# Kernel tuning notes

Hardware: AMD Instinct MI355X
Metric: run time of the kernel (lower is better)

## Reference

```python
import math
import jax, jax.numpy as jnp
import numpy as np

ANCHORS_SETTINGS = (
    dict(layer='p3', stride=32, size=48, scale=[2 ** (1.0 / 3.0), 2 ** (2.0 / 3.0)], aspect_ratio=[0.667, 1, 1.5]),
    dict(layer='p4', stride=64, size=96, scale=[2 ** (1.0 / 3.0), 2 ** (2.0 / 3.0)], aspect_ratio=[0.667, 1, 1.5]),
    dict(layer='p5', stride=128, size=192, scale=[1, 2 ** (1.0 / 3.0), 2 ** (2.0 / 3.0)], aspect_ratio=[0.667, 1, 1.5]),
)


def anchor_configs():
    # 21 static (kernel, stride, padding) configs, in the exact counter order of
    # weighted_anchor_aggregator (p3 x6, p4 x6, p5 x9).
    cfgs = []
    for info in ANCHORS_SETTINGS:
        stride, size = info['stride'], info['size']
        for scale in info['scale']:
            for ar in info['aspect_ratio']:
                kernel = (int(size * scale / float(ar) ** 0.5), int(size * scale * float(ar) ** 0.5))
                padding = (math.ceil((kernel[0] - stride) / 2.0), math.ceil((kernel[1] - stride) / 2.0))
                cfgs.append((kernel, (stride, stride), padding))
    return cfgs


def extract_weighted_patches(x, weights, kernel, stride, padding):
    # x: (B,H,W,C); weights: (B,k,gh,gw). Vectorized equivalent of the original
    # lax.scan over per-position dynamic_slice gathers:
    #   acc = sum_{i,j} weights[:,:,i,j] (x) x_pad[:, i*s : i*s+kh, j*s : j*s+kw, :]
    b = x.shape[0]
    _, k, gh, gw = weights.shape
    xp = jnp.pad(x, ((0, 0),
                     (padding[0], padding[0] + kernel[0]),
                     (padding[1], padding[1] + kernel[1]),
                     (0, 0)))
    rows = jnp.arange(gh)[:, None] * stride[0] + jnp.arange(kernel[0])[None, :]  # (gh, kh)
    cols = jnp.arange(gw)[:, None] * stride[1] + jnp.arange(kernel[1])[None, :]  # (gw, kw)
    # gather all strided patches: (B, gh, kh, gw, kw, C)
    patches = xp[:, rows][:, :, :, cols]
    # weighted sum over grid positions -> (B, k, kh, kw, C)
    return jnp.einsum('bkij,bihjwc->bkhwc', weights, patches)


def _aggregate(x, weights_p3, weights_p4, weights_p5):
    weights = ([weights_p3[:, a] for a in range(weights_p3.shape[1])]
               + [weights_p4[:, a] for a in range(weights_p4.shape[1])]
               + [weights_p5[:, a] for a in range(weights_p5.shape[1])])
    b, k = weights[0].shape[0], weights[0].shape[1]
    acc = jnp.zeros((b * k, 224, 224, 3), x.dtype)
    for w, (kernel, stride, padding) in zip(weights, anchor_configs()):
        agg = extract_weighted_patches(x, w, kernel, stride, padding)
        agg = agg.reshape(b * k, kernel[0], kernel[1], 3)
        acc = acc + jax.image.resize(agg, (b * k, 224, 224, 3), 'bilinear')
    return acc


def setup_inputs() -> dict:
    key = jax.random.key(0)
    k0, k1, k2, k3 = jax.random.split(key, 4)
    B, K = 8, 4
    return {
        'x': jax.random.normal(k0, (B, 448, 448, 3), jnp.float32),
        'weights_p3': jax.random.uniform(k1, (B, 6, K, 14, 14), jnp.float32),
        'weights_p4': jax.random.uniform(k2, (B, 6, K, 7, 7), jnp.float32),
        'weights_p5': jax.random.uniform(k3, (B, 9, K, 4, 4), jnp.float32),
    }


def reference(x, weights_p3, weights_p4, weights_p5):
    return _aggregate(x, weights_p3, weights_p4, weights_p5)
```

## Files before the change

kernel.cpp:

```cpp
#include <hip/hip_runtime.h>
#include <math.h>


#define BATCH 8
#define KK 4
#define OUT_HW 224
#define IMG_HW 448
#define NCFG 21

#define WTBL_BYTES (NCFG * 2 * OUT_HW * 16)
#define ITBL_BYTES (NCFG * 2 * OUT_HW * 4)
#define WT_OFF_BYTES (WTBL_BYTES + ITBL_BYTES)
#define WT_F4 12912
#define AGG_OFF_BYTES (WT_OFF_BYTES + WT_F4 * 16)

#define RZ_GRID (14 * 14 * 16)

typedef float v2f __attribute__((ext_vector_type(2)));

static constexpr int cKH[NCFG]  = {74,60,49,93,76,62, 148,120,98,186,152,124,
                                   235,192,156,296,241,197,373,304,248};
static constexpr int cKW[NCFG]  = {49,60,74,62,76,93, 98,120,148,124,152,186,
                                   156,192,235,197,241,296,248,304,373};
static constexpr int cMTH[NCFG] = {2,2,2,2,2,2, 2,2,2,2,2,2, 3,2,2,3,3,2,4,3,3};
static constexpr int cMTW[NCFG] = {2,2,2,2,2,2, 2,2,2,2,2,2, 2,2,3,2,3,3,3,3,4};

__host__ __device__ constexpr int ckwp(int c) { return cKW[c] + (cKW[c] & 1); }
__host__ __device__ constexpr long cwsoff(int c, int g) {
    long o = 0;
    for (int k = g; k < c; ++k) o += (long)cKH[k] * ckwp(k) * (BATCH * KK);
    return o;
}

struct ACfg {
    int kh, kw, kwp, p0, p1;
    int layer;
    int ns;
    int wt_off;
    int ws_off;
    int block_start;
    int blocks_per_img;
};

struct AggArgs {
    ACfg e[NCFG];
    int n;
};

struct TablesArgs { int kh[NCFG]; int kw[NCFG]; };

struct TrArgs {
    int layer[NCFG];
    int anchor[NCFG];
    int gsz[NCFG];
    int wt_off[NCFG];
};

struct F3 { float a, b, c; };

__device__ inline unsigned int bf16_rne(float f) {
    unsigned int u = __float_as_uint(f);
    return (u + 0x7fffu + ((u >> 16) & 1u)) >> 16;
}

__global__ __launch_bounds__(256) void init_tables(float4* __restrict__ wtbl,
                                                   int* __restrict__ itbl,
                                                   TablesArgs t) {
    int cfg = blockIdx.x >> 1;
    int dim = blockIdx.x & 1;
    int o = threadIdx.x;
    if (o >= OUT_HW) return;
    int n = dim ? t.kw[cfg] : t.kh[cfg];

    float inv = (float)(1.0 / ((double)OUT_HW / (double)n));
    float ks  = inv > 1.f ? inv : 1.f;
    float rks = 1.f / ks;
    float sf  = ((float)o + 0.5f) * inv - 0.5f;
    int i0 = (int)ceilf(sf - ks);  if (i0 < 0) i0 = 0;
    int i1 = (int)floorf(sf + ks); if (i1 > n - 1) i1 = n - 1;
    float sum = 0.f;
    for (int i = i0; i <= i1; ++i) {
        float v = 1.f - fabsf((float)i - sf) * rks;
        sum += (v > 0.f ? v : 0.f);
    }
    float rsum = 1.f / sum;
    float w[4];
#pragma unroll
    for (int d = 0; d < 4; ++d) {
        int i = i0 + d;
        float v = 0.f;
        if (i <= i1) {
            v = 1.f - fabsf((float)i - sf) * rks;
            v = (v > 0.f ? v : 0.f) * rsum;
        }
        w[d] = v;
    }
    int idx = cfg * (2 * OUT_HW) + dim * OUT_HW + o;
    wtbl[idx] = make_float4(w[0], w[1], w[2], w[3]);
    itbl[idx] = i0;
}

__global__ __launch_bounds__(256) void transpose_w(
        const float* __restrict__ wp3, const float* __restrict__ wp4,
        const float* __restrict__ wp5, float4* __restrict__ wT, TrArgs t) {
    int cfg = blockIdx.x;
    int b = blockIdx.y;
    int gsz = t.gsz[cfg];
    const float* base;
    int A;
    if (t.layer[cfg] == 0)      { base = wp3; A = 6; }
    else if (t.layer[cfg] == 1) { base = wp4; A = 6; }
    else                        { base = wp5; A = 9; }
    const float* src = base + (size_t)(b * A + t.anchor[cfg]) * (KK * gsz);
    for (int g = threadIdx.x; g < gsz; g += 256) {
        wT[t.wt_off[cfg] + b * gsz + g] =
            make_float4(src[0 * gsz + g], src[1 * gsz + g],
                        src[2 * gsz + g], src[3 * gsz + g]);
    }
}

template <int GH, int GW, int STRIDE, int L2S>
__device__ inline void agg_body(const ACfg& c, int b, int h, int slot,
                                const float* __restrict__ xb,
                                const float4* __restrict__ wlds,
                                uint2* __restrict__ agg) {
    const int w0 = (((slot >> L2S) << (L2S + 1)) | (slot & (STRIDE - 1)));
    const int w1 = w0 + STRIDE;
    const bool two = w1 < c.kw;

    v2f acc2[4][3];
#pragma unroll
    for (int k = 0; k < 4; ++k)
#pragma unroll
        for (int ch = 0; ch < 3; ++ch) { acc2[k][ch].x = 0.f; acc2[k][ch].y = 0.f; }

    const int rb = h - c.p0;
    int ilo = rb >= 0 ? 0 : (-rb + STRIDE - 1) / STRIDE;
    int ihi = (IMG_HW - 1 - rb) / STRIDE;
    if (ihi > GH - 1) ihi = GH - 1;

    const int cb = w0 - c.p1;

    int  cof[GW + 1];
    bool ok [GW + 1];
#pragma unroll
    for (int jj = 0; jj <= GW; ++jj) {
        int col = cb + jj * STRIDE;
        ok[jj] = (unsigned)col < (unsigned)IMG_HW;
        unsigned cc = (unsigned)col;
        if (cc > (unsigned)(IMG_HW - 1)) cc = (unsigned)(IMG_HW - 1);
        cof[jj] = (int)cc * 3;
    }

#pragma unroll 1
    for (int i = ilo; i <= ihi; ++i) {
        const float* xr = xb + (size_t)(rb + i * STRIDE) * (IMG_HW * 3);
        const float4* wrow = wlds + i * GW;

        float px[GW + 1][3];
#pragma unroll
        for (int jj = 0; jj <= GW; ++jj) {
            F3 v = *(const F3*)(xr + cof[jj]);
            px[jj][0] = ok[jj] ? v.a : 0.f;
            px[jj][1] = ok[jj] ? v.b : 0.f;
            px[jj][2] = ok[jj] ? v.c : 0.f;
        }

#pragma unroll
        for (int j = 0; j < GW; ++j) {
            float4 wk = wrow[j];
            v2f d0 = {px[j][0], px[j + 1][0]};
            v2f d1 = {px[j][1], px[j + 1][1]};
            v2f d2 = {px[j][2], px[j + 1][2]};
            v2f wv0 = {wk.x, wk.x};
            v2f wv1 = {wk.y, wk.y};
            v2f wv2 = {wk.z, wk.z};
            v2f wv3 = {wk.w, wk.w};
            acc2[0][0] = __builtin_elementwise_fma(wv0, d0, acc2[0][0]);
            acc2[0][1] = __builtin_elementwise_fma(wv0, d1, acc2[0][1]);
            acc2[0][2] = __builtin_elementwise_fma(wv0, d2, acc2[0][2]);
            acc2[1][0] = __builtin_elementwise_fma(wv1, d0, acc2[1][0]);
            acc2[1][1] = __builtin_elementwise_fma(wv1, d1, acc2[1][1]);
            acc2[1][2] = __builtin_elementwise_fma(wv1, d2, acc2[1][2]);
            acc2[2][0] = __builtin_elementwise_fma(wv2, d0, acc2[2][0]);
            acc2[2][1] = __builtin_elementwise_fma(wv2, d1, acc2[2][1]);
            acc2[2][2] = __builtin_elementwise_fma(wv2, d2, acc2[2][2]);
            acc2[3][0] = __builtin_elementwise_fma(wv3, d0, acc2[3][0]);
            acc2[3][1] = __builtin_elementwise_fma(wv3, d1, acc2[3][1]);
            acc2[3][2] = __builtin_elementwise_fma(wv3, d2, acc2[3][2]);
        }
    }

    const int npix = c.kh * c.kwp;
    size_t pb0 = (size_t)c.ws_off
               + ((size_t)b * npix + (size_t)h * c.kwp + w0) * KK;
    {
        uint4 s0, s1;
        s0.x = bf16_rne(acc2[0][0].x) | (bf16_rne(acc2[0][1].x) << 16);
        s0.y = bf16_rne(acc2[0][2].x);
        s0.z = bf16_rne(acc2[1][0].x) | (bf16_rne(acc2[1][1].x) << 16);
        s0.w = bf16_rne(acc2[1][2].x);
        s1.x = bf16_rne(acc2[2][0].x) | (bf16_rne(acc2[2][1].x) << 16);
        s1.y = bf16_rne(acc2[2][2].x);
        s1.z = bf16_rne(acc2[3][0].x) | (bf16_rne(acc2[3][1].x) << 16);
        s1.w = bf16_rne(acc2[3][2].x);
        *(uint4*)(agg + pb0)     = s0;
        *(uint4*)(agg + pb0 + 2) = s1;
    }
    if (two) {
        size_t pb1 = pb0 + (size_t)STRIDE * KK;
        uint4 s0, s1;
        s0.x = bf16_rne(acc2[0][0].y) | (bf16_rne(acc2[0][1].y) << 16);
        s0.y = bf16_rne(acc2[0][2].y);
        s0.z = bf16_rne(acc2[1][0].y) | (bf16_rne(acc2[1][1].y) << 16);
        s0.w = bf16_rne(acc2[1][2].y);
        s1.x = bf16_rne(acc2[2][0].y) | (bf16_rne(acc2[2][1].y) << 16);
        s1.y = bf16_rne(acc2[2][2].y);
        s1.z = bf16_rne(acc2[3][0].y) | (bf16_rne(acc2[3][1].y) << 16);
        s1.w = bf16_rne(acc2[3][2].y);
        *(uint4*)(agg + pb1)     = s0;
        *(uint4*)(agg + pb1 + 2) = s1;
    }
}

__device__ inline void agg_top(int bid, const float* __restrict__ x,
                               const float4* __restrict__ wT,
                               uint2* __restrict__ agg, const AggArgs& a,
                               float4* wlds, int tid) {
    int ci = 0;
    while (ci + 1 < a.n && bid >= a.e[ci + 1].block_start) ci++;
    const ACfg c = a.e[ci];
    int local = bid - c.block_start;
    int b     = local & 7;
    int sblk  = local >> 3;

    const int gsz = (c.layer == 0) ? 196 : (c.layer == 1) ? 49 : 16;
    for (int t = tid; t < gsz; t += 256)
        wlds[t] = wT[c.wt_off + b * gsz + t];
    __syncthreads();

    int pidx = sblk * 256 + tid;
    if (pidx >= c.kh * c.ns) return;
    int h    = pidx / c.ns;
    int slot = pidx - h * c.ns;

    const float* __restrict__ xb = x + (size_t)b * (IMG_HW * IMG_HW * 3);
    if (c.layer == 0)      agg_body<14, 14, 32, 5>(c, b, h, slot, xb, wlds, agg);
    else if (c.layer == 1) agg_body<7, 7, 64, 6>(c, b, h, slot, xb, wlds, agg);
    else                   agg_body<4, 4, 128, 7>(c, b, h, slot, xb, wlds, agg);
}

__global__ __launch_bounds__(256, 3) void agg_all(
        const float* __restrict__ x,
        const float4* __restrict__ wT,
        uint2* __restrict__ agg,
        AggArgs a) {
    __shared__ float4 wlds[196];
    agg_top(blockIdx.x, x, wT, agg, a, wlds, (int)threadIdx.x);
}

template <int TH, int TW, int KH_, int KW_, int KWP_>
__device__ inline void taps_ct2(const uint2* __restrict__ pb,
                                int i0, int j0,
                                float4 wh4, float4 ww4,
                                v2f (&a)[3]) {
    const float* wh = (const float*)&wh4;
    const float* ww = (const float*)&ww4;
    uint4 v[TH][TW];
#pragma unroll
    for (int d = 0; d < TH; ++d) {
        int gi = i0 + d;
        if (gi > KH_ - 1) gi = KH_ - 1;
        const uint2* rp = pb + (size_t)gi * (KWP_ * KK);
#pragma unroll
        for (int e = 0; e < TW; ++e) {
            int gj = j0 + e;
            if (gj > KW_ - 1) gj = KW_ - 1;
            v[d][e] = *(const uint4*)(rp + gj * KK);
        }
    }
#pragma unroll
    for (int d = 0; d < TH; ++d) {
        v2f r0 = {0.f, 0.f}, r1 = {0.f, 0.f}, r2 = {0.f, 0.f};
#pragma unroll
        for (int e = 0; e < TW; ++e) {
            uint4 q = v[d][e];
            v2f c0, c1, c2;
            c0.x = __uint_as_float(q.x << 16);
            c0.y = __uint_as_float(q.z << 16);
            c1.x = __uint_as_float(q.x & 0xffff0000u);
            c1.y = __uint_as_float(q.z & 0xffff0000u);
            c2.x = __uint_as_float(q.y << 16);
            c2.y = __uint_as_float(q.w << 16);
            v2f w2 = {ww[e], ww[e]};
            r0 = __builtin_elementwise_fma(w2, c0, r0);
            r1 = __builtin_elementwise_fma(w2, c1, r1);
            r2 = __builtin_elementwise_fma(w2, c2, r2);
        }
        v2f h2 = {wh[d], wh[d]};
        a[0] = __builtin_elementwise_fma(h2, r0, a[0]);
        a[1] = __builtin_elementwise_fma(h2, r1, a[1]);
        a[2] = __builtin_elementwise_fma(h2, r2, a[2]);
    }
}

template <int C, int CEND, int CSTART>
__device__ inline void do_rounds(const uint2* __restrict__ agg,
                                 const float4* __restrict__ wlds,
                                 const int* __restrict__ ilds,
                                 int b, int kp, int tx, int ty,
                                 v2f (&a)[3]) {
    if constexpr (C < CEND) {
        constexpr int li  = C - CSTART;
        constexpr int kh  = cKH[C];
        constexpr int kw  = cKW[C];
        constexpr int kwp = ckwp(C);
        constexpr long wso = cwsoff(C, CSTART);
        float4 wh4 = wlds[li * 32 + ty];
        float4 ww4 = wlds[li * 32 + 16 + tx];
        int i0 = ilds[li * 32 + ty];
        int j0 = ilds[li * 32 + 16 + tx];
        const uint2* pb = agg + wso
                        + (size_t)b * ((size_t)kh * kwp * KK) + kp * 2;
        taps_ct2<cMTH[C], cMTW[C], kh, kw, kwp>(pb, i0, j0, wh4, ww4, a);
        do_rounds<C + 1, CEND, CSTART>(agg, wlds, ilds, b, kp, tx, ty, a);
    }
}

template <int CSTART, int CEND>
__device__ inline void rz_top(const uint2* __restrict__ agg,
                              const float4* __restrict__ wtbl,
                              const int* __restrict__ itbl,
                              float* __restrict__ out, int accumulate,
                              int bx, int by, int zz, int tid,
                              float4* wlds, int* ilds) {
    constexpr int NC = CEND - CSTART;
    const int tx = tid & 15;
    const int ty = tid >> 4;
    const int xo = bx * 16 + tx;
    const int yo = by * 16 + ty;
    const int b  = zz >> 1;
    const int kp = zz & 1;

    for (int e = tid; e < NC * 32; e += 256) {
        int ci  = e >> 5;
        int r   = e & 31;
        int isW = r >> 4;
        int idx = r & 15;
        int base_o = isW ? (bx * 16) : (by * 16);
        int src = (CSTART + ci) * (2 * OUT_HW) + isW * OUT_HW + base_o + idx;
        wlds[ci * 32 + r] = wtbl[src];
        ilds[ci * 32 + r] = itbl[src];
    }
    __syncthreads();

    size_t obA = ((((size_t)(b * KK + kp * 2)) * OUT_HW + yo) * OUT_HW + xo) * 3;
    size_t obB = obA + (size_t)OUT_HW * OUT_HW * 3;

    v2f a[3];
    if (accumulate) {
        a[0].x = out[obA + 0]; a[0].y = out[obB + 0];
        a[1].x = out[obA + 1]; a[1].y = out[obB + 1];
        a[2].x = out[obA + 2]; a[2].y = out[obB + 2];
    } else {
        a[0] = v2f{0.f, 0.f}; a[1] = v2f{0.f, 0.f}; a[2] = v2f{0.f, 0.f};
    }

    do_rounds<CSTART, CEND, CSTART>(agg, wlds, ilds, b, kp, tx, ty, a);

    out[obA + 0] = a[0].x; out[obA + 1] = a[1].x; out[obA + 2] = a[2].x;
    out[obB + 0] = a[0].y; out[obB + 1] = a[1].y; out[obB + 2] = a[2].y;
}

template <int CSTART, int CEND>
__global__ __launch_bounds__(256, 4) void resize_static(
        const uint2* __restrict__ agg,
        const float4* __restrict__ wtbl,
        const int* __restrict__ itbl,
        float* __restrict__ out,
        int accumulate) {
    constexpr int NC = CEND - CSTART;
    __shared__ float4 wlds[NC * 32];
    __shared__ int    ilds[NC * 32];
    rz_top<CSTART, CEND>(agg, wtbl, itbl, out, accumulate,
                         (int)blockIdx.x, (int)blockIdx.y, (int)blockIdx.z,
                         (int)threadIdx.x, wlds, ilds);
}

template <int CSTART, int CEND>
__global__ __launch_bounds__(256, 3) void fused_k(
        const float* __restrict__ x,
        const float4* __restrict__ wT,
        uint2* __restrict__ aggW,
        AggArgs a, int naggBlocks,
        const uint2* __restrict__ aggR,
        const float4* __restrict__ wtbl,
        const int* __restrict__ itbl,
        float* __restrict__ out,
        int accumulate) {
    constexpr int NC = CEND - CSTART;
    __shared__ float4 wldsA[196];
    __shared__ float4 wldsR[NC * 32];
    __shared__ int    ildsR[NC * 32];
    const int tid = (int)threadIdx.x;
    if ((int)blockIdx.x < naggBlocks) {
        agg_top((int)blockIdx.x, x, wT, aggW, a, wldsA, tid);
    } else {
        int rid = (int)blockIdx.x - naggBlocks;
        int bx = rid % 14;
        int t2 = rid / 14;
        int by = t2 % 14;
        int zz = t2 / 14;
        rz_top<CSTART, CEND>(aggR, wtbl, itbl, out, accumulate,
                             bx, by, zz, tid, wldsR, ildsR);
    }
}

extern "C" void kernel_launch(void* const* d_in, const int* in_sizes, int n_in,
                              void* d_out, int out_size, void* d_ws, size_t ws_size,
                              hipStream_t stream) {
    const float* x   = (const float*)d_in[0];
    const float* wp3 = (const float*)d_in[1];
    const float* wp4 = (const float*)d_in[2];
    const float* wp5 = (const float*)d_in[3];
    float* out = (float*)d_out;
    float4* wtbl = (float4*)d_ws;
    int*    itbl = (int*)((char*)d_ws + WTBL_BYTES);
    float4* wT   = (float4*)((char*)d_ws + WT_OFF_BYTES);
    uint2*  agg  = (uint2*)((char*)d_ws + AGG_OFF_BYTES);

    struct { int stride, size, nscale; double scales[3]; int gh; } layers[3] = {
        {32, 48, 2, {pow(2.0, 1.0 / 3.0), pow(2.0, 2.0 / 3.0), 0.0}, 14},
        {64, 96, 2, {pow(2.0, 1.0 / 3.0), pow(2.0, 2.0 / 3.0), 0.0}, 7},
        {128, 192, 3, {1.0, pow(2.0, 1.0 / 3.0), pow(2.0, 2.0 / 3.0)}, 4},
    };
    const double ars[3] = {0.667, 1.0, 1.5};

    struct HostCfg {
        int kh, kw, kwp, stride, p0, p1, gh, gw, layer, anchor, wt_off;
        int ns, blocks_per_img;
    } cfg[NCFG];
    TablesArgs ta;
    TrArgs tr;
    int nc = 0, wt_run = 0;
    for (int L = 0; L < 3; ++L) {
        int anchor = 0;
        for (int si = 0; si < layers[L].nscale; ++si) {
            for (int ai = 0; ai < 3; ++ai) {
                double ss = (double)layers[L].size * layers[L].scales[si];
                double sq = pow(ars[ai], 0.5);
                int kh = (int)(ss / sq);
                int kw = (int)(ss * sq);
                HostCfg& e = cfg[nc];
                e.kh = kh; e.kw = kw;
                e.kwp = kw + (kw & 1);
                e.stride = layers[L].stride;
                e.p0 = (int)ceil((double)(kh - layers[L].stride) / 2.0);
                e.p1 = (int)ceil((double)(kw - layers[L].stride) / 2.0);
                e.gh = layers[L].gh; e.gw = layers[L].gh;
                e.layer = L; e.anchor = anchor++;
                int s = e.stride;
                int q = kw / s, r = kw % s;
                e.ns = ((q + 1) / 2) * s + ((q % 2 == 0) ? r : 0);
                e.blocks_per_img = (kh * e.ns + 255) / 256;
                e.wt_off = wt_run;
                int gsz = e.gh * e.gw;
                wt_run += BATCH * gsz;
                ta.kh[nc] = kh; ta.kw[nc] = kw;
                tr.layer[nc] = L; tr.anchor[nc] = e.anchor;
                tr.gsz[nc] = gsz; tr.wt_off[nc] = e.wt_off;
                ++nc;
            }
        }
    }

    init_tables<<<NCFG * 2, 256, 0, stream>>>(wtbl, itbl, ta);
    transpose_w<<<dim3(NCFG, BATCH), 256, 0, stream>>>(wp3, wp4, wp5, wT, tr);

    auto build = [&](int gstart, int gend, AggArgs& aa) -> int {
        aa.n = 0;
        int ablocks = 0;
        size_t off = 0;
        for (int c = gstart; c < gend; ++c) {
            ACfg& lc = aa.e[aa.n++];
            lc.kh = cfg[c].kh; lc.kw = cfg[c].kw; lc.kwp = cfg[c].kwp;
            lc.p0 = cfg[c].p0; lc.p1 = cfg[c].p1;
            lc.layer = cfg[c].layer;
            lc.ns = cfg[c].ns;
            lc.wt_off = cfg[c].wt_off;
            lc.ws_off = (int)off;
            lc.block_start = ablocks;
            lc.blocks_per_img = cfg[c].blocks_per_img;
            ablocks += cfg[c].blocks_per_img * BATCH;
            off += (size_t)cfg[c].kh * cfg[c].kwp * (BATCH * KK);
        }
        return ablocks;
    };
    auto gpx = [&](int gstart, int gend) -> size_t {
        size_t p = 0;
        for (int c = gstart; c < gend; ++c)
            p += (size_t)cfg[c].kh * cfg[c].kwp;
        return p * (BATCH * KK);
    };

    size_t pxH = gpx(12, 15), px1 = gpx(0, 12), px2 = gpx(15, 19),
           px3 = gpx(19, 21);
    size_t pxA = pxH > px2 ? pxH : px2;
    size_t pxB = px1 > px3 ? px1 : px3;
    bool can_overlap =
        (size_t)AGG_OFF_BYTES + (pxA + pxB) * sizeof(uint2) <= ws_size;

    dim3 rgrid(14, 14, 16);

    if (can_overlap) {
        uint2* bufA = agg;
        uint2* bufB = agg + pxA;
        AggArgs aH, a1, a2, a3;
        int nH = build(12, 15, aH);
        int n1 = build(0, 12, a1);
        int n2 = build(15, 19, a2);
        int n3 = build(19, 21, a3);

        agg_all<<<nH, 256, 0, stream>>>(x, wT, bufA, aH);
        fused_k<12, 15><<<n1 + RZ_GRID, 256, 0, stream>>>(
            x, wT, bufB, a1, n1, bufA, wtbl, itbl, out, 0);
        fused_k<0, 12><<<n2 + RZ_GRID, 256, 0, stream>>>(
            x, wT, bufA, a2, n2, bufB, wtbl, itbl, out, 1);
        fused_k<15, 19><<<n3 + RZ_GRID, 256, 0, stream>>>(
            x, wT, bufB, a3, n3, bufA, wtbl, itbl, out, 1);
        resize_static<19, 21><<<rgrid, 256, 0, stream>>>(
            bufB, wtbl, itbl, out, 1);
    } else {
        AggArgs aa;
        int nb;
        nb = build(12, 15, aa);
        agg_all<<<nb, 256, 0, stream>>>(x, wT, agg, aa);
        resize_static<12, 15><<<rgrid, 256, 0, stream>>>(agg, wtbl, itbl, out, 0);
        nb = build(0, 12, aa);
        agg_all<<<nb, 256, 0, stream>>>(x, wT, agg, aa);
        resize_static<0, 12><<<rgrid, 256, 0, stream>>>(agg, wtbl, itbl, out, 1);
        nb = build(15, 19, aa);
        agg_all<<<nb, 256, 0, stream>>>(x, wT, agg, aa);
        resize_static<15, 19><<<rgrid, 256, 0, stream>>>(agg, wtbl, itbl, out, 1);
        nb = build(19, 21, aa);
        agg_all<<<nb, 256, 0, stream>>>(x, wT, agg, aa);
        resize_static<19, 21><<<rgrid, 256, 0, stream>>>(agg, wtbl, itbl, out, 1);
    }
    (void)in_sizes; (void)n_in; (void)out_size;
}
```

Baseline: 273.6 us.

## Register-block two output rows per thread to reuse image row loads

Each thread now computes two output rows, h0 and h0+stride, in addition to the two columns it already handled. Input rows shared between those outputs are loaded once and combined with two shifted weight rows. The weight table in LDS is padded with zero rows above and below so boundary rows need no special case. This roughly halves global image loads and the number of threads. In exchange it doubles accumulator registers, which may reduce occupancy, and leaves fewer blocks to schedule.

```diff
diff --git a/kernel.cpp b/kernel.cpp
--- a/kernel.cpp
+++ b/kernel.cpp
@@ -15,6 +15,7 @@
 #define AGG_OFF_BYTES (WT_OFF_BYTES + WT_F4 * 16)
 
 #define RZ_GRID (14 * 14 * 16)
+#define WPAD_MAX 224
 
 typedef float v2f __attribute__((ext_vector_type(2)));
 
@@ -36,6 +37,7 @@
     int kh, kw, kwp, p0, p1;
     int layer;
     int ns;
+    int nsh;
     int wt_off;
     int ws_off;
     int block_start;
@@ -120,24 +122,30 @@
 }
 
 template <int GH, int GW, int STRIDE, int L2S>
-__device__ inline void agg_body(const ACfg& c, int b, int h, int slot,
+__device__ inline void agg_body(const ACfg& c, int b, int hs, int ws,
                                 const float* __restrict__ xb,
                                 const float4* __restrict__ wlds,
                                 uint2* __restrict__ agg) {
-    const int w0 = (((slot >> L2S) << (L2S + 1)) | (slot & (STRIDE - 1)));
-    const int w1 = w0 + STRIDE;
-    const bool two = w1 < c.kw;
-
-    v2f acc2[4][3];
-#pragma unroll
-    for (int k = 0; k < 4; ++k)
-#pragma unroll
-        for (int ch = 0; ch < 3; ++ch) { acc2[k][ch].x = 0.f; acc2[k][ch].y = 0.f; }
-
-    const int rb = h - c.p0;
-    int ilo = rb >= 0 ? 0 : (-rb + STRIDE - 1) / STRIDE;
-    int ihi = (IMG_HW - 1 - rb) / STRIDE;
-    if (ihi > GH - 1) ihi = GH - 1;
+    const int w0 = ((ws >> L2S) << (L2S + 1)) | (ws & (STRIDE - 1));
+    const bool two_w = (w0 + STRIDE) < c.kw;
+    const int h0 = ((hs >> L2S) << (L2S + 1)) | (hs & (STRIDE - 1));
+    const bool two_h = (h0 + STRIDE) < c.kh;
+
+    v2f acc2[2][4][3];
+#pragma unroll
+    for (int hh = 0; hh < 2; ++hh)
+#pragma unroll
+        for (int k = 0; k < 4; ++k)
+#pragma unroll
+            for (int ch = 0; ch < 3; ++ch) {
+                acc2[hh][k][ch].x = 0.f; acc2[hh][k][ch].y = 0.f;
+            }
+
+    const int rb = h0 - c.p0;
+    int mlo = rb >= 0 ? 0 : (-rb + STRIDE - 1) / STRIDE;
+    int mhi = (IMG_HW - 1 - rb) / STRIDE;
+    int mcap = two_h ? GH : GH - 1;
+    if (mhi > mcap) mhi = mcap;
 
     const int cb = w0 - c.p1;
 
@@ -153,9 +161,10 @@
     }
 
 #pragma unroll 1
-    for (int i = ilo; i <= ihi; ++i) {
-        const float* xr = xb + (size_t)(rb + i * STRIDE) * (IMG_HW * 3);
-        const float4* wrow = wlds + i * GW;
+    for (int m = mlo; m <= mhi; ++m) {
+        const float* xr = xb + (size_t)(rb + m * STRIDE) * (IMG_HW * 3);
+        const float4* wr0 = wlds + (m + 1) * GW;
+        const float4* wr1 = wlds + m * GW;
 
         float px[GW + 1][3];
 #pragma unroll
@@ -168,58 +177,84 @@
 
 #pragma unroll
         for (int j = 0; j < GW; ++j) {
-            float4 wk = wrow[j];
             v2f d0 = {px[j][0], px[j + 1][0]};
             v2f d1 = {px[j][1], px[j + 1][1]};
             v2f d2 = {px[j][2], px[j + 1][2]};
-            v2f wv0 = {wk.x, wk.x};
-            v2f wv1 = {wk.y, wk.y};
-            v2f wv2 = {wk.z, wk.z};
-            v2f wv3 = {wk.w, wk.w};
-            acc2[0][0] = __builtin_elementwise_fma(wv0, d0, acc2[0][0]);
-            acc2[0][1] = __builtin_elementwise_fma(wv0, d1, acc2[0][1]);
-            acc2[0][2] = __builtin_elementwise_fma(wv0, d2, acc2[0][2]);
-            acc2[1][0] = __builtin_elementwise_fma(wv1, d0, acc2[1][0]);
-            acc2[1][1] = __builtin_elementwise_fma(wv1, d1, acc2[1][1]);
-            acc2[1][2] = __builtin_elementwise_fma(wv1, d2, acc2[1][2]);
-            acc2[2][0] = __builtin_elementwise_fma(wv2, d0, acc2[2][0]);
-            acc2[2][1] = __builtin_elementwise_fma(wv2, d1, acc2[2][1]);
-            acc2[2][2] = __builtin_elementwise_fma(wv2, d2, acc2[2][2]);
-            acc2[3][0] = __builtin_elementwise_fma(wv3, d0, acc2[3][0]);
-            acc2[3][1] = __builtin_elementwise_fma(wv3, d1, acc2[3][1]);
-            acc2[3][2] = __builtin_elementwise_fma(wv3, d2, acc2[3][2]);
+            float4 wk0 = wr0[j];
+            float4 wk1 = wr1[j];
+            {
+                v2f wv0 = {wk0.x, wk0.x};
+                v2f wv1 = {wk0.y, wk0.y};
+                v2f wv2 = {wk0.z, wk0.z};
+                v2f wv3 = {wk0.w, wk0.w};
+                acc2[0][0][0] = __builtin_elementwise_fma(wv0, d0, acc2[0][0][0]);
+                acc2[0][0][1] = __builtin_elementwise_fma(wv0, d1, acc2[0][0][1]);
+                acc2[0][0][2] = __builtin_elementwise_fma(wv0, d2, acc2[0][0][2]);
+                acc2[0][1][0] = __builtin_elementwise_fma(wv1, d0, acc2[0][1][0]);
+                acc2[0][1][1] = __builtin_elementwise_fma(wv1, d1, acc2[0][1][1]);
+                acc2[0][1][2] = __builtin_elementwise_fma(wv1, d2, acc2[0][1][2]);
+                acc2[0][2][0] = __builtin_elementwise_fma(wv2, d0, acc2[0][2][0]);
+                acc2[0][2][1] = __builtin_elementwise_fma(wv2, d1, acc2[0][2][1]);
+                acc2[0][2][2] = __builtin_elementwise_fma(wv2, d2, acc2[0][2][2]);
+                acc2[0][3][0] = __builtin_elementwise_fma(wv3, d0, acc2[0][3][0]);
+                acc2[0][3][1] = __builtin_elementwise_fma(wv3, d1, acc2[0][3][1]);
+                acc2[0][3][2] = __builtin_elementwise_fma(wv3, d2, acc2[0][3][2]);
+            }
+            {
+                v2f wv0 = {wk1.x, wk1.x};
+                v2f wv1 = {wk1.y, wk1.y};
+                v2f wv2 = {wk1.z, wk1.z};
+                v2f wv3 = {wk1.w, wk1.w};
+                acc2[1][0][0] = __builtin_elementwise_fma(wv0, d0, acc2[1][0][0]);
+                acc2[1][0][1] = __builtin_elementwise_fma(wv0, d1, acc2[1][0][1]);
+                acc2[1][0][2] = __builtin_elementwise_fma(wv0, d2, acc2[1][0][2]);
+                acc2[1][1][0] = __builtin_elementwise_fma(wv1, d0, acc2[1][1][0]);
+                acc2[1][1][1] = __builtin_elementwise_fma(wv1, d1, acc2[1][1][1]);
+                acc2[1][1][2] = __builtin_elementwise_fma(wv1, d2, acc2[1][1][2]);
+                acc2[1][2][0] = __builtin_elementwise_fma(wv2, d0, acc2[1][2][0]);
+                acc2[1][2][1] = __builtin_elementwise_fma(wv2, d1, acc2[1][2][1]);
+                acc2[1][2][2] = __builtin_elementwise_fma(wv2, d2, acc2[1][2][2]);
+                acc2[1][3][0] = __builtin_elementwise_fma(wv3, d0, acc2[1][3][0]);
+                acc2[1][3][1] = __builtin_elementwise_fma(wv3, d1, acc2[1][3][1]);
+                acc2[1][3][2] = __builtin_elementwise_fma(wv3, d2, acc2[1][3][2]);
+            }
         }
     }
 
     const int npix = c.kh * c.kwp;
-    size_t pb0 = (size_t)c.ws_off
-               + ((size_t)b * npix + (size_t)h * c.kwp + w0) * KK;
-    {
-        uint4 s0, s1;
-        s0.x = bf16_rne(acc2[0][0].x) | (bf16_rne(acc2[0][1].x) << 16);
-        s0.y = bf16_rne(acc2[0][2].x);
-        s0.z = bf16_rne(acc2[1][0].x) | (bf16_rne(acc2[1][1].x) << 16);
-        s0.w = bf16_rne(acc2[1][2].x);
-        s1.x = bf16_rne(acc2[2][0].x) | (bf16_rne(acc2[2][1].x) << 16);
-        s1.y = bf16_rne(acc2[2][2].x);
-        s1.z = bf16_rne(acc2[3][0].x) | (bf16_rne(acc2[3][1].x) << 16);
-        s1.w = bf16_rne(acc2[3][2].x);
-        *(uint4*)(agg + pb0)     = s0;
-        *(uint4*)(agg + pb0 + 2) = s1;
-    }
-    if (two) {
-        size_t pb1 = pb0 + (size_t)STRIDE * KK;
-        uint4 s0, s1;
-        s0.x = bf16_rne(acc2[0][0].y) | (bf16_rne(acc2[0][1].y) << 16);
-        s0.y = bf16_rne(acc2[0][2].y);
-        s0.z = bf16_rne(acc2[1][0].y) | (bf16_rne(acc2[1][1].y) << 16);
-        s0.w = bf16_rne(acc2[1][2].y);
-        s1.x = bf16_rne(acc2[2][0].y) | (bf16_rne(acc2[2][1].y) << 16);
-        s1.y = bf16_rne(acc2[2][2].y);
-        s1.z = bf16_rne(acc2[3][0].y) | (bf16_rne(acc2[3][1].y) << 16);
-        s1.w = bf16_rne(acc2[3][2].y);
-        *(uint4*)(agg + pb1)     = s0;
-        *(uint4*)(agg + pb1 + 2) = s1;
+#pragma unroll
+    for (int hh = 0; hh < 2; ++hh) {
+        if (hh == 1 && !two_h) break;
+        int h = h0 + hh * STRIDE;
+        size_t pb0 = (size_t)c.ws_off
+                   + ((size_t)b * npix + (size_t)h * c.kwp + w0) * KK;
+        {
+            uint4 s0, s1;
+            s0.x = bf16_rne(acc2[hh][0][0].x) | (bf16_rne(acc2[hh][0][1].x) << 16);
+            s0.y = bf16_rne(acc2[hh][0][2].x);
+            s0.z = bf16_rne(acc2[hh][1][0].x) | (bf16_rne(acc2[hh][1][1].x) << 16);
+            s0.w = bf16_rne(acc2[hh][1][2].x);
+            s1.x = bf16_rne(acc2[hh][2][0].x) | (bf16_rne(acc2[hh][2][1].x) << 16);
+            s1.y = bf16_rne(acc2[hh][2][2].x);
+            s1.z = bf16_rne(acc2[hh][3][0].x) | (bf16_rne(acc2[hh][3][1].x) << 16);
+            s1.w = bf16_rne(acc2[hh][3][2].x);
+            *(uint4*)(agg + pb0)     = s0;
+            *(uint4*)(agg + pb0 + 2) = s1;
+        }
+        if (two_w) {
+            size_t pb1 = pb0 + (size_t)STRIDE * KK;
+            uint4 s0, s1;
+            s0.x = bf16_rne(acc2[hh][0][0].y) | (bf16_rne(acc2[hh][0][1].y) << 16);
+            s0.y = bf16_rne(acc2[hh][0][2].y);
+            s0.z = bf16_rne(acc2[hh][1][0].y) | (bf16_rne(acc2[hh][1][1].y) << 16);
+            s0.w = bf16_rne(acc2[hh][1][2].y);
+            s1.x = bf16_rne(acc2[hh][2][0].y) | (bf16_rne(acc2[hh][2][1].y) << 16);
+            s1.y = bf16_rne(acc2[hh][2][2].y);
+            s1.z = bf16_rne(acc2[hh][3][0].y) | (bf16_rne(acc2[hh][3][1].y) << 16);
+            s1.w = bf16_rne(acc2[hh][3][2].y);
+            *(uint4*)(agg + pb1)     = s0;
+            *(uint4*)(agg + pb1 + 2) = s1;
+        }
     }
 }
 
@@ -234,20 +269,28 @@
     int b     = local & 7;
     int sblk  = local >> 3;
 
-    const int gsz = (c.layer == 0) ? 196 : (c.layer == 1) ? 49 : 16;
-    for (int t = tid; t < gsz; t += 256)
-        wlds[t] = wT[c.wt_off + b * gsz + t];
+    const int gh = (c.layer == 0) ? 14 : (c.layer == 1) ? 7 : 4;
+    const int gsz = gh * gh;
+    const int gszp = (gh + 2) * gh;
+    for (int t = tid; t < gszp; t += 256) {
+        int r = t / gh;
+        int cc = t - r * gh;
+        float4 v = make_float4(0.f, 0.f, 0.f, 0.f);
+        if (r >= 1 && r <= gh)
+            v = wT[c.wt_off + b * gsz + (r - 1) * gh + cc];
+        wlds[t] = v;
+    }
     __syncthreads();
 
     int pidx = sblk * 256 + tid;
-    if (pidx >= c.kh * c.ns) return;
-    int h    = pidx / c.ns;
-    int slot = pidx - h * c.ns;
+    if (pidx >= c.nsh * c.ns) return;
+    int hs = pidx / c.ns;
+    int ws = pidx - hs * c.ns;
 
     const float* __restrict__ xb = x + (size_t)b * (IMG_HW * IMG_HW * 3);
-    if (c.layer == 0)      agg_body<14, 14, 32, 5>(c, b, h, slot, xb, wlds, agg);
-    else if (c.layer == 1) agg_body<7, 7, 64, 6>(c, b, h, slot, xb, wlds, agg);
-    else                   agg_body<4, 4, 128, 7>(c, b, h, slot, xb, wlds, agg);
+    if (c.layer == 0)      agg_body<14, 14, 32, 5>(c, b, hs, ws, xb, wlds, agg);
+    else if (c.layer == 1) agg_body<7, 7, 64, 6>(c, b, hs, ws, xb, wlds, agg);
+    else                   agg_body<4, 4, 128, 7>(c, b, hs, ws, xb, wlds, agg);
 }
 
 __global__ __launch_bounds__(256, 3) void agg_all(
@@ -255,7 +298,7 @@
         const float4* __restrict__ wT,
         uint2* __restrict__ agg,
         AggArgs a) {
-    __shared__ float4 wlds[196];
+    __shared__ float4 wlds[WPAD_MAX];
     agg_top(blockIdx.x, x, wT, agg, a, wlds, (int)threadIdx.x);
 }
 
@@ -399,7 +442,7 @@
         float* __restrict__ out,
         int accumulate) {
     constexpr int NC = CEND - CSTART;
-    __shared__ float4 wldsA[196];
+    __shared__ float4 wldsA[WPAD_MAX];
     __shared__ float4 wldsR[NC * 32];
     __shared__ int    ildsR[NC * 32];
     const int tid = (int)threadIdx.x;
@@ -438,7 +481,7 @@
 
     struct HostCfg {
         int kh, kw, kwp, stride, p0, p1, gh, gw, layer, anchor, wt_off;
-        int ns, blocks_per_img;
+        int ns, nsh, blocks_per_img;
     } cfg[NCFG];
     TablesArgs ta;
     TrArgs tr;
@@ -460,9 +503,15 @@
                 e.gh = layers[L].gh; e.gw = layers[L].gh;
                 e.layer = L; e.anchor = anchor++;
                 int s = e.stride;
-                int q = kw / s, r = kw % s;
-                e.ns = ((q + 1) / 2) * s + ((q % 2 == 0) ? r : 0);
-                e.blocks_per_img = (kh * e.ns + 255) / 256;
+                {
+                    int q = kw / s, r = kw % s;
+                    e.ns = ((q + 1) / 2) * s + ((q % 2 == 0) ? r : 0);
+                }
+                {
+                    int q = kh / s, r = kh % s;
+                    e.nsh = ((q + 1) / 2) * s + ((q % 2 == 0) ? r : 0);
+                }
+                e.blocks_per_img = (e.nsh * e.ns + 255) / 256;
                 e.wt_off = wt_run;
                 int gsz = e.gh * e.gw;
                 wt_run += BATCH * gsz;
@@ -487,6 +536,7 @@
             lc.p0 = cfg[c].p0; lc.p1 = cfg[c].p1;
             lc.layer = cfg[c].layer;
             lc.ns = cfg[c].ns;
+            lc.nsh = cfg[c].nsh;
             lc.wt_off = cfg[c].wt_off;
             lc.ws_off = (int)off;
             lc.block_start = ablocks;
```

Measured after the change: 283.7 us. +3.7%, slower.

## Process all four k-channels per resize thread with 32x8 output tiles

Applied to the files above, without the earlier changes.

Each resize thread now produces all four k outputs for one pixel instead of two, loading two adjacent uint4 per tap and accumulating in 4-wide vectors. Block tiles change from 16x16 to 32x8 on a flattened grid, with a matching change to the LDS weight/index table layout. This halves the resize thread count and reuses the tap index and weight math across more channels. In exchange it raises register pressure (double the tap buffers), which could lower occupancy.

```diff
diff --git a/kernel.cpp b/kernel.cpp
--- a/kernel.cpp
+++ b/kernel.cpp
@@ -14,9 +14,11 @@
 #define WT_F4 12912
 #define AGG_OFF_BYTES (WT_OFF_BYTES + WT_F4 * 16)
 
-#define RZ_GRID (14 * 14 * 16)
+#define RZ_GRID (7 * 28 * 8)
+#define TBL_STRIDE 40
 
 typedef float v2f __attribute__((ext_vector_type(2)));
+typedef float v4f __attribute__((ext_vector_type(4)));
 
 static constexpr int cKH[NCFG]  = {74,60,49,93,76,62, 148,120,98,186,152,124,
                                    235,192,156,296,241,197,373,304,248};
@@ -260,13 +262,13 @@
 }
 
 template <int TH, int TW, int KH_, int KW_, int KWP_>
-__device__ inline void taps_ct2(const uint2* __restrict__ pb,
+__device__ inline void taps_ct4(const uint2* __restrict__ pb,
                                 int i0, int j0,
                                 float4 wh4, float4 ww4,
-                                v2f (&a)[3]) {
+                                v4f (&a)[3]) {
     const float* wh = (const float*)&wh4;
     const float* ww = (const float*)&ww4;
-    uint4 v[TH][TW];
+    uint4 v0[TH][TW], v1[TH][TW];
 #pragma unroll
     for (int d = 0; d < TH; ++d) {
         int gi = i0 + d;
@@ -276,31 +278,41 @@
         for (int e = 0; e < TW; ++e) {
             int gj = j0 + e;
             if (gj > KW_ - 1) gj = KW_ - 1;
-            v[d][e] = *(const uint4*)(rp + gj * KK);
+            v0[d][e] = *(const uint4*)(rp + gj * KK);
+            v1[d][e] = *(const uint4*)(rp + gj * KK + 2);
         }
     }
 #pragma unroll
     for (int d = 0; d < TH; ++d) {
-        v2f r0 = {0.f, 0.f}, r1 = {0.f, 0.f}, r2 = {0.f, 0.f};
+        v4f r0 = {0.f, 0.f, 0.f, 0.f};
+        v4f r1 = {0.f, 0.f, 0.f, 0.f};
+        v4f r2 = {0.f, 0.f, 0.f, 0.f};
 #pragma unroll
         for (int e = 0; e < TW; ++e) {
-            uint4 q = v[d][e];
-            v2f c0, c1, c2;
-            c0.x = __uint_as_float(q.x << 16);
-            c0.y = __uint_as_float(q.z << 16);
-            c1.x = __uint_as_float(q.x & 0xffff0000u);
-            c1.y = __uint_as_float(q.z & 0xffff0000u);
-            c2.x = __uint_as_float(q.y << 16);
-            c2.y = __uint_as_float(q.w << 16);
-            v2f w2 = {ww[e], ww[e]};
-            r0 = __builtin_elementwise_fma(w2, c0, r0);
-            r1 = __builtin_elementwise_fma(w2, c1, r1);
-            r2 = __builtin_elementwise_fma(w2, c2, r2);
-        }
-        v2f h2 = {wh[d], wh[d]};
-        a[0] = __builtin_elementwise_fma(h2, r0, a[0]);
-        a[1] = __builtin_elementwise_fma(h2, r1, a[1]);
-        a[2] = __builtin_elementwise_fma(h2, r2, a[2]);
+            uint4 qa = v0[d][e];
+            uint4 qb = v1[d][e];
+            v4f c0, c1, c2;
+            c0.x = __uint_as_float(qa.x << 16);
+            c0.y = __uint_as_float(qa.z << 16);
+            c0.z = __uint_as_float(qb.x << 16);
+            c0.w = __uint_as_float(qb.z << 16);
+            c1.x = __uint_as_float(qa.x & 0xffff0000u);
+            c1.y = __uint_as_float(qa.z & 0xffff0000u);
+            c1.z = __uint_as_float(qb.x & 0xffff0000u);
+            c1.w = __uint_as_float(qb.z & 0xffff0000u);
+            c2.x = __uint_as_float(qa.y << 16);
+            c2.y = __uint_as_float(qa.w << 16);
+            c2.z = __uint_as_float(qb.y << 16);
+            c2.w = __uint_as_float(qb.w << 16);
+            v4f w4 = {ww[e], ww[e], ww[e], ww[e]};
+            r0 = __builtin_elementwise_fma(w4, c0, r0);
+            r1 = __builtin_elementwise_fma(w4, c1, r1);
+            r2 = __builtin_elementwise_fma(w4, c2, r2);
+        }
+        v4f h4 = {wh[d], wh[d], wh[d], wh[d]};
+        a[0] = __builtin_elementwise_fma(h4, r0, a[0]);
+        a[1] = __builtin_elementwise_fma(h4, r1, a[1]);
+        a[2] = __builtin_elementwise_fma(h4, r2, a[2]);
     }
 }
 
@@ -308,22 +320,21 @@
 __device__ inline void do_rounds(const uint2* __restrict__ agg,
                                  const float4* __restrict__ wlds,
                                  const int* __restrict__ ilds,
-                                 int b, int kp, int tx, int ty,
-                                 v2f (&a)[3]) {
+                                 int b, int tx, int ty,
+                                 v4f (&a)[3]) {
     if constexpr (C < CEND) {
         constexpr int li  = C - CSTART;
         constexpr int kh  = cKH[C];
         constexpr int kw  = cKW[C];
         constexpr int kwp = ckwp(C);
         constexpr long wso = cwsoff(C, CSTART);
-        float4 wh4 = wlds[li * 32 + ty];
-        float4 ww4 = wlds[li * 32 + 16 + tx];
-        int i0 = ilds[li * 32 + ty];
-        int j0 = ilds[li * 32 + 16 + tx];
-        const uint2* pb = agg + wso
-                        + (size_t)b * ((size_t)kh * kwp * KK) + kp * 2;
-        taps_ct2<cMTH[C], cMTW[C], kh, kw, kwp>(pb, i0, j0, wh4, ww4, a);
-        do_rounds<C + 1, CEND, CSTART>(agg, wlds, ilds, b, kp, tx, ty, a);
+        float4 wh4 = wlds[li * TBL_STRIDE + ty];
+        float4 ww4 = wlds[li * TBL_STRIDE + 8 + tx];
+        int i0 = ilds[li * TBL_STRIDE + ty];
+        int j0 = ilds[li * TBL_STRIDE + 8 + tx];
+        const uint2* pb = agg + wso + (size_t)b * ((size_t)kh * kwp * KK);
+        taps_ct4<cMTH[C], cMTW[C], kh, kw, kwp>(pb, i0, j0, wh4, ww4, a);
+        do_rounds<C + 1, CEND, CSTART>(agg, wlds, ilds, b, tx, ty, a);
     }
 }
 
@@ -332,44 +343,61 @@
                               const float4* __restrict__ wtbl,
                               const int* __restrict__ itbl,
                               float* __restrict__ out, int accumulate,
-                              int bx, int by, int zz, int tid,
+                              int bx, int by, int b, int tid,
                               float4* wlds, int* ilds) {
     constexpr int NC = CEND - CSTART;
-    const int tx = tid & 15;
-    const int ty = tid >> 4;
-    const int xo = bx * 16 + tx;
-    const int yo = by * 16 + ty;
-    const int b  = zz >> 1;
-    const int kp = zz & 1;
-
-    for (int e = tid; e < NC * 32; e += 256) {
-        int ci  = e >> 5;
-        int r   = e & 31;
-        int isW = r >> 4;
-        int idx = r & 15;
-        int base_o = isW ? (bx * 16) : (by * 16);
-        int src = (CSTART + ci) * (2 * OUT_HW) + isW * OUT_HW + base_o + idx;
-        wlds[ci * 32 + r] = wtbl[src];
-        ilds[ci * 32 + r] = itbl[src];
+    const int tx = tid & 31;
+    const int ty = tid >> 5;
+    const int xo = bx * 32 + tx;
+    const int yo = by * 8 + ty;
+
+    for (int e = tid; e < NC * TBL_STRIDE; e += 256) {
+        int ci  = e / TBL_STRIDE;
+        int r   = e - ci * TBL_STRIDE;
+        int isW = r >= 8;
+        int idx = isW ? (r - 8) : r;
+        int base_o = isW ? (bx * 32) : (by * 8);
+        int src = (CSTART + ci) * (2 * OUT_HW) + (isW ? OUT_HW : 0)
+                + base_o + idx;
+        wlds[ci * TBL_STRIDE + r] = wtbl[src];
+        ilds[ci * TBL_STRIDE + r] = itbl[src];
     }
     __syncthreads();
 
-    size_t obA = ((((size_t)(b * KK + kp * 2)) * OUT_HW + yo) * OUT_HW + xo) * 3;
-    size_t obB = obA + (size_t)OUT_HW * OUT_HW * 3;
-
-    v2f a[3];
+    const size_t plane = (size_t)OUT_HW * OUT_HW * 3;
+    size_t ob0 = ((((size_t)(b * KK)) * OUT_HW + yo) * OUT_HW + xo) * 3;
+
+    v4f a[3];
     if (accumulate) {
-        a[0].x = out[obA + 0]; a[0].y = out[obB + 0];
-        a[1].x = out[obA + 1]; a[1].y = out[obB + 1];
-        a[2].x = out[obA + 2]; a[2].y = out[obB + 2];
+#pragma unroll
+        for (int ch = 0; ch < 3; ++ch) {
+            a[ch].x = out[ob0 + 0 * plane + ch];
+            a[ch].y = out[ob0 + 1 * plane + ch];
+            a[ch].z = out[ob0 + 2 * plane + ch];
+            a[ch].w = out[ob0 + 3 * plane + ch];
+        }
     } else {
-        a[0] = v2f{0.f, 0.f}; a[1] = v2f{0.f, 0.f}; a[2] = v2f{0.f, 0.f};
-    }
-
-    do_rounds<CSTART, CEND, CSTART>(agg, wlds, ilds, b, kp, tx, ty, a);
-
-    out[obA + 0] = a[0].x; out[obA + 1] = a[1].x; out[obA + 2] = a[2].x;
-    out[obB + 0] = a[0].y; out[obB + 1] = a[1].y; out[obB + 2] = a[2].y;
+#pragma unroll
+        for (int ch = 0; ch < 3; ++ch)
+            a[ch] = v4f{0.f, 0.f, 0.f, 0.f};
+    }
+
+    do_rounds<CSTART, CEND, CSTART>(agg, wlds, ilds, b, tx, ty, a);
+
+#pragma unroll
+    for (int ch = 0; ch < 3; ++ch) {
+        out[ob0 + 0 * plane + ch] = a[ch].x;
+        out[ob0 + 1 * plane + ch] = a[ch].y;
+        out[ob0 + 2 * plane + ch] = a[ch].z;
+        out[ob0 + 3 * plane + ch] = a[ch].w;
+    }
+}
+
+__device__ inline void rz_decomp(int rid, int& bx, int& by, int& b) {
+    bx = rid % 7;
+    int t2 = rid / 7;
+    by = t2 % 28;
+    b  = t2 / 28;
 }
 
 template <int CSTART, int CEND>
@@ -380,11 +408,12 @@
         float* __restrict__ out,
         int accumulate) {
     constexpr int NC = CEND - CSTART;
-    __shared__ float4 wlds[NC * 32];
-    __shared__ int    ilds[NC * 32];
+    __shared__ float4 wlds[NC * TBL_STRIDE];
+    __shared__ int    ilds[NC * TBL_STRIDE];
+    int bx, by, b;
+    rz_decomp((int)blockIdx.x, bx, by, b);
     rz_top<CSTART, CEND>(agg, wtbl, itbl, out, accumulate,
-                         (int)blockIdx.x, (int)blockIdx.y, (int)blockIdx.z,
-                         (int)threadIdx.x, wlds, ilds);
+                         bx, by, b, (int)threadIdx.x, wlds, ilds);
 }
 
 template <int CSTART, int CEND>
@@ -400,19 +429,16 @@
         int accumulate) {
     constexpr int NC = CEND - CSTART;
     __shared__ float4 wldsA[196];
-    __shared__ float4 wldsR[NC * 32];
-    __shared__ int    ildsR[NC * 32];
+    __shared__ float4 wldsR[NC * TBL_STRIDE];
+    __shared__ int    ildsR[NC * TBL_STRIDE];
     const int tid = (int)threadIdx.x;
     if ((int)blockIdx.x < naggBlocks) {
         agg_top((int)blockIdx.x, x, wT, aggW, a, wldsA, tid);
     } else {
-        int rid = (int)blockIdx.x - naggBlocks;
-        int bx = rid % 14;
-        int t2 = rid / 14;
-        int by = t2 % 14;
-        int zz = t2 / 14;
+        int bx, by, b;
+        rz_decomp((int)blockIdx.x - naggBlocks, bx, by, b);
         rz_top<CSTART, CEND>(aggR, wtbl, itbl, out, accumulate,
-                             bx, by, zz, tid, wldsR, ildsR);
+                             bx, by, b, tid, wldsR, ildsR);
     }
 }
 
@@ -510,8 +536,6 @@
     bool can_overlap =
         (size_t)AGG_OFF_BYTES + (pxA + pxB) * sizeof(uint2) <= ws_size;
 
-    dim3 rgrid(14, 14, 16);
-
     if (can_overlap) {
         uint2* bufA = agg;
         uint2* bufB = agg + pxA;
@@ -528,23 +552,23 @@
             x, wT, bufA, a2, n2, bufB, wtbl, itbl, out, 1);
         fused_k<15, 19><<<n3 + RZ_GRID, 256, 0, stream>>>(
             x, wT, bufB, a3, n3, bufA, wtbl, itbl, out, 1);
-        resize_static<19, 21><<<rgrid, 256, 0, stream>>>(
+        resize_static<19, 21><<<RZ_GRID, 256, 0, stream>>>(
             bufB, wtbl, itbl, out, 1);
     } else {
         AggArgs aa;
         int nb;
         nb = build(12, 15, aa);
         agg_all<<<nb, 256, 0, stream>>>(x, wT, agg, aa);
-        resize_static<12, 15><<<rgrid, 256, 0, stream>>>(agg, wtbl, itbl, out, 0);
+        resize_static<12, 15><<<RZ_GRID, 256, 0, stream>>>(agg, wtbl, itbl, out, 0);
         nb = build(0, 12, aa);
         agg_all<<<nb, 256, 0, stream>>>(x, wT, agg, aa);
-        resize_static<0, 12><<<rgrid, 256, 0, stream>>>(agg, wtbl, itbl, out, 1);
+        resize_static<0, 12><<<RZ_GRID, 256, 0, stream>>>(agg, wtbl, itbl, out, 1);
         nb = build(15, 19, aa);
         agg_all<<<nb, 256, 0, stream>>>(x, wT, agg, aa);
-        resize_static<15, 19><<<rgrid, 256, 0, stream>>>(agg, wtbl, itbl, out, 1);
+        resize_static<15, 19><<<RZ_GRID, 256, 0, stream>>>(agg, wtbl, itbl, out, 1);
         nb = build(19, 21, aa);
         agg_all<<<nb, 256, 0, stream>>>(x, wT, agg, aa);
-        resize_static<19, 21><<<rgrid, 256, 0, stream>>>(agg, wtbl, itbl, out, 1);
+        resize_static<19, 21><<<RZ_GRID, 256, 0, stream>>>(agg, wtbl, itbl, out, 1);
     }
     (void)in_sizes; (void)n_in; (void)out_size;
 }
```

Result: no change. 272.6 us (-0.4%).
